# Optimization experiments

Measured on AMD Instinct MI355X. Metric: run time of the kernel, lower is better.

## Reference

```python
import jax, jax.numpy as jnp
import numpy as np

B, S, E, H, DK, DV, DF = 4, 2048, 512, 8, 64, 64, 2048
EPS = 1e-3  # keras LayerNormalization default epsilon


def setup_inputs() -> dict:
    key = jax.random.key(0)
    ks = jax.random.split(key, 24)
    def n(k, shape, scale=0.02):
        return jax.random.normal(k, shape, jnp.float32) * scale
    inp = {}
    inp["x"] = jax.random.normal(ks[0], (B, S, E), jnp.float32)
    inp["encoder_output"] = jax.random.normal(ks[1], (B, S, E), jnp.float32)
    # lookahead mask: 1 above the diagonal (masked), broadcast over batch/heads
    inp["lookahead_mask"] = jnp.triu(jnp.ones((S, S), jnp.int32), k=1)[None, None]
    # padding mask: 0 = keep (no padding in this synthetic batch)
    inp["padding_mask"] = jnp.zeros((B, 1, 1, S), jnp.int32)
    # self-attention params
    inp["sa_Wq"] = n(ks[2], (E, H * DK)); inp["sa_bq"] = jnp.zeros((H * DK,), jnp.float32)
    inp["sa_Wk"] = n(ks[3], (E, H * DK)); inp["sa_bk"] = jnp.zeros((H * DK,), jnp.float32)
    inp["sa_Wv"] = n(ks[4], (E, H * DV)); inp["sa_bv"] = jnp.zeros((H * DV,), jnp.float32)
    inp["sa_Wo"] = n(ks[5], (H * DV, E)); inp["sa_bo"] = jnp.zeros((E,), jnp.float32)
    # cross-attention params
    inp["ca_Wq"] = n(ks[6], (E, H * DK)); inp["ca_bq"] = jnp.zeros((H * DK,), jnp.float32)
    inp["ca_Wk"] = n(ks[7], (E, H * DK)); inp["ca_bk"] = jnp.zeros((H * DK,), jnp.float32)
    inp["ca_Wv"] = n(ks[8], (E, H * DV)); inp["ca_bv"] = jnp.zeros((H * DV,), jnp.float32)
    inp["ca_Wo"] = n(ks[9], (H * DV, E)); inp["ca_bo"] = jnp.zeros((E,), jnp.float32)
    # feed-forward params
    inp["ff_W1"] = n(ks[10], (E, DF)); inp["ff_b1"] = jnp.zeros((DF,), jnp.float32)
    inp["ff_W2"] = n(ks[11], (DF, E)); inp["ff_b2"] = jnp.zeros((E,), jnp.float32)
    # layernorm params (3 add&norm blocks)
    for i in (1, 2, 3):
        inp[f"ln{i}_g"] = jnp.ones((E,), jnp.float32)
        inp[f"ln{i}_b"] = jnp.zeros((E,), jnp.float32)
    return inp


def _mha(q_in, k_in, v_in, mask, Wq, bq, Wk, bk, Wv, bv, Wo, bo):
    Bq, Sq, _ = q_in.shape
    Sk = k_in.shape[1]
    q = (q_in @ Wq + bq).reshape(Bq, Sq, H, DK).transpose(0, 2, 1, 3)  # bhqd
    k = (k_in @ Wk + bk).reshape(Bq, Sk, H, DK).transpose(0, 2, 1, 3)  # bhkd
    v = (v_in @ Wv + bv).reshape(Bq, Sk, H, DV).transpose(0, 2, 1, 3)  # bhkd
    scores = jnp.einsum("bhqd,bhkd->bhqk", q, k) / jnp.sqrt(jnp.float32(DK))
    scores = scores - 1e9 * mask.astype(scores.dtype)  # additive mask (1 = masked)
    attn = jax.nn.softmax(scores, axis=-1)
    out = jnp.einsum("bhqk,bhkd->bhqd", attn, v)
    out = out.transpose(0, 2, 1, 3).reshape(Bq, Sq, H * DV)
    return out @ Wo + bo


def _add_norm(x, sub, g, b):
    y = x + sub
    m = jnp.mean(y, axis=-1, keepdims=True)
    v = jnp.var(y, axis=-1, keepdims=True)
    return (y - m) / jnp.sqrt(v + EPS) * g + b


def reference(x, encoder_output, lookahead_mask, padding_mask,
              sa_Wq, sa_bq, sa_Wk, sa_bk, sa_Wv, sa_bv, sa_Wo, sa_bo,
              ca_Wq, ca_bq, ca_Wk, ca_bk, ca_Wv, ca_bv, ca_Wo, ca_bo,
              ff_W1, ff_b1, ff_W2, ff_b2,
              ln1_g, ln1_b, ln2_g, ln2_b, ln3_g, ln3_b):
    # dropout is identity at inference (training=False)
    a1 = _mha(x, x, x, lookahead_mask,
              sa_Wq, sa_bq, sa_Wk, sa_bk, sa_Wv, sa_bv, sa_Wo, sa_bo)
    x1 = _add_norm(x, a1, ln1_g, ln1_b)
    a2 = _mha(x1, encoder_output, encoder_output, padding_mask,
              ca_Wq, ca_bq, ca_Wk, ca_bk, ca_Wv, ca_bv, ca_Wo, ca_bo)
    x2 = _add_norm(x1, a2, ln2_g, ln2_b)
    ff = jax.nn.relu(x2 @ ff_W1 + ff_b1) @ ff_W2 + ff_b2
    return _add_norm(x2, ff, ln3_g, ln3_b)
```

## Files before the change

kernel.cpp:

```cpp
#include <hip/hip_runtime.h>

#define Bx  4
#define Sx  2048
#define Ex  512
#define Hx  8
#define Tt  (Bx * Sx)

typedef short          short8 __attribute__((ext_vector_type(8)));
typedef float          f32x4  __attribute__((ext_vector_type(4)));
typedef unsigned short u16;

__device__ __forceinline__ u16 f2bf(float f) {
    unsigned int u = __float_as_uint(f);
    u += 0x7fffu + ((u >> 16) & 1u);
    return (u16)(u >> 16);
}
__device__ __forceinline__ float bf2f(u16 h) {
    return __uint_as_float(((unsigned int)h) << 16);
}
__device__ __forceinline__ unsigned int cvt_pk_bf16(float lo, float hi) {
    unsigned int r;
    asm("v_cvt_pk_bf16_f32 %0, %1, %2" : "=v"(r) : "v"(lo), "v"(hi));
    return r;
}
typedef const __attribute__((address_space(1))) void* gas1_t;
typedef __attribute__((address_space(3))) void*       las3_t;
__device__ __forceinline__ void gload16(const u16* g, u16* l) {
    __builtin_amdgcn_global_load_lds((gas1_t)g, (las3_t)l, 16, 0, 0);
}

__global__ __launch_bounds__(256) void f32_to_bf16_2(const float* __restrict__ a,
                                                     const float* __restrict__ b,
                                                     u16* __restrict__ oa,
                                                     u16* __restrict__ ob)
{
    const float* in  = blockIdx.y ? b : a;
    u16*         out = blockIdx.y ? ob : oa;
    int i = (blockIdx.x * 256 + threadIdx.x) << 2;
    float4 v = *(const float4*)(in + i);
    ushort4 o;
    o.x = f2bf(v.x); o.y = f2bf(v.y); o.z = f2bf(v.z); o.w = f2bf(v.w);
    *(ushort4*)(out + i) = o;
}

__global__ __launch_bounds__(256) void transpose_bf16(const float* __restrict__ W,
                                                      u16* __restrict__ Wt,
                                                      int K, int N)
{
    __shared__ u16 tile[32][33];
    const int n0 = blockIdx.x * 32, k0 = blockIdx.y * 32;
    const int tx = threadIdx.x & 31, ty = threadIdx.x >> 5;
#pragma unroll
    for (int i = 0; i < 32; i += 8)
        tile[ty + i][tx] = f2bf(W[(size_t)(k0 + ty + i) * N + n0 + tx]);
    __syncthreads();
#pragma unroll
    for (int i = 0; i < 32; i += 8)
        Wt[(size_t)(n0 + ty + i) * K + k0 + tx] = tile[tx][ty + i];
}

struct WPtrs { const float* w[8]; };
__global__ __launch_bounds__(256) void transpose8_bf16(WPtrs ws, u16* __restrict__ base)
{
    __shared__ u16 tile[32][33];
    const float* W  = ws.w[blockIdx.z];
    u16*         Wt = base + (size_t)blockIdx.z * 262144;
    const int n0 = blockIdx.x * 32, k0 = blockIdx.y * 32;
    const int tx = threadIdx.x & 31, ty = threadIdx.x >> 5;
#pragma unroll
    for (int i = 0; i < 32; i += 8)
        tile[ty + i][tx] = f2bf(W[(size_t)(k0 + ty + i) * 512 + n0 + tx]);
    __syncthreads();
#pragma unroll
    for (int i = 0; i < 32; i += 8)
        Wt[(size_t)(n0 + ty + i) * 512 + k0 + tx] = tile[tx][ty + i];
}

template<int OUT_BF16, int RELU>
__global__ __launch_bounds__(256) void gemm128(const u16* __restrict__ A,
                                               const u16* __restrict__ Bt,
                                               const float* __restrict__ b0,
                                               const float* __restrict__ b1,
                                               const float* __restrict__ b2,
                                               const float* __restrict__ b3,
                                               void* __restrict__ Cout,
                                               int M, int N, int K, int ldc)
{
    __shared__ u16 As[128 * 32];
    __shared__ u16 Bs[128 * 32];

    const int tid  = threadIdx.x;
    const int w    = tid >> 6;
    const int lane = tid & 63;
    const int c    = lane & 15;
    const int quad = lane >> 4;
    const int wr   = w >> 1, wc = w & 1;
    const int m0   = blockIdx.y * 128;
    const int n0   = blockIdx.x * 128;

    const int srow = lane >> 2;
    const int scol = (lane & 3) << 3;
    const u16* Ag0 = A  + (size_t)(m0 + w * 32 + srow) * K + scol;
    const u16* Ag1 = Ag0 + (size_t)16 * K;
    const u16* Bg0 = Bt + (size_t)(n0 + w * 32 + srow) * K + scol;
    const u16* Bg1 = Bg0 + (size_t)16 * K;
    u16* AsB0 = &As[(w * 2 + 0) * 512];
    u16* AsB1 = &As[(w * 2 + 1) * 512];
    u16* BsB0 = &Bs[(w * 2 + 0) * 512];
    u16* BsB1 = &Bs[(w * 2 + 1) * 512];

    f32x4 acc[4][4];
#pragma unroll
    for (int i = 0; i < 4; i++)
#pragma unroll
        for (int j = 0; j < 4; j++) { acc[i][j][0]=0.f; acc[i][j][1]=0.f; acc[i][j][2]=0.f; acc[i][j][3]=0.f; }

    for (int k0 = 0; k0 < K; k0 += 32) {
        __syncthreads();
        gload16(Ag0 + k0, AsB0);
        gload16(Ag1 + k0, AsB1);
        gload16(Bg0 + k0, BsB0);
        gload16(Bg1 + k0, BsB1);
        __syncthreads();

        short8 af[4], bf[4];
#pragma unroll
        for (int i = 0; i < 4; i++)
            af[i] = *(const short8*)&As[(wr * 64 + i * 16 + c) * 32 + quad * 8];
#pragma unroll
        for (int j = 0; j < 4; j++)
            bf[j] = *(const short8*)&Bs[(wc * 64 + j * 16 + c) * 32 + quad * 8];
#pragma unroll
        for (int i = 0; i < 4; i++)
#pragma unroll
            for (int j = 0; j < 4; j++)
                acc[i][j] = __builtin_amdgcn_mfma_f32_16x16x32_bf16(af[i], bf[j], acc[i][j], 0, 0, 0);
    }

    const int seg = n0 >> 9;
    const float* bp = seg == 0 ? b0 : (seg == 1 ? b1 : (seg == 2 ? b2 : b3));
    const int nbase = n0 & 511;
    float bv[4];
#pragma unroll
    for (int j = 0; j < 4; j++) bv[j] = bp[nbase + wc * 64 + j * 16 + c];

#pragma unroll
    for (int i = 0; i < 4; i++) {
#pragma unroll
        for (int j = 0; j < 4; j++) {
            int colg = n0 + wc * 64 + j * 16 + c;
#pragma unroll
            for (int r = 0; r < 4; r++) {
                int rowg = m0 + wr * 64 + i * 16 + quad * 4 + r;
                float v = acc[i][j][r] + bv[j];
                if (RELU) v = fmaxf(v, 0.f);
                if (OUT_BF16) ((u16*)Cout)[(size_t)rowg * ldc + colg] = f2bf(v);
                else          ((float*)Cout)[(size_t)rowg * ldc + colg] = v;
            }
        }
    }
}

template<int OUT_BF16, int RELU>
__global__ __launch_bounds__(128) void gemm64(const u16* __restrict__ A,
                                              const u16* __restrict__ Bt,
                                              const float* __restrict__ bias,
                                              void* __restrict__ Cout,
                                              int M, int N, int K, int ldc)
{
    __shared__ u16 As[128 * 40];
    __shared__ u16 Bs[64 * 40];

    const int tid  = threadIdx.x;
    const int w    = tid >> 6;
    const int lane = tid & 63;
    const int c    = lane & 15;
    const int quad = lane >> 4;
    const int m0   = blockIdx.y * 128;
    const int n0   = blockIdx.x * 64;

    const int rA = tid >> 2;
    const int kc = (tid & 3) << 3;

    const u16* Ap = A  + (size_t)(m0 + rA) * K + kc;
    const u16* Bp = Bt + (size_t)(n0 + rA) * K + kc;
    const size_t a32 = (size_t)32 * K;

    f32x4 acc[4][4];
#pragma unroll
    for (int i = 0; i < 4; i++)
#pragma unroll
        for (int j = 0; j < 4; j++) { acc[i][j][0]=0.f; acc[i][j][1]=0.f; acc[i][j][2]=0.f; acc[i][j][3]=0.f; }

    short8 ra[4], rb[2];
#pragma unroll
    for (int i = 0; i < 4; i++) ra[i] = *(const short8*)(Ap + i * a32);
#pragma unroll
    for (int i = 0; i < 2; i++) rb[i] = *(const short8*)(Bp + i * a32);

    for (int k0 = 0; k0 < K; k0 += 32) {
        __syncthreads();
#pragma unroll
        for (int i = 0; i < 4; i++) *(short8*)&As[(rA + i * 32) * 40 + kc] = ra[i];
#pragma unroll
        for (int i = 0; i < 2; i++) *(short8*)&Bs[(rA + i * 32) * 40 + kc] = rb[i];
        __syncthreads();

        if (k0 + 32 < K) {
#pragma unroll
            for (int i = 0; i < 4; i++) ra[i] = *(const short8*)(Ap + i * a32 + k0 + 32);
#pragma unroll
            for (int i = 0; i < 2; i++) rb[i] = *(const short8*)(Bp + i * a32 + k0 + 32);
        }

        short8 af[4], bf[4];
#pragma unroll
        for (int i = 0; i < 4; i++)
            af[i] = *(const short8*)&As[(w * 64 + i * 16 + c) * 40 + quad * 8];
#pragma unroll
        for (int j = 0; j < 4; j++)
            bf[j] = *(const short8*)&Bs[(j * 16 + c) * 40 + quad * 8];
#pragma unroll
        for (int i = 0; i < 4; i++)
#pragma unroll
            for (int j = 0; j < 4; j++)
                acc[i][j] = __builtin_amdgcn_mfma_f32_16x16x32_bf16(af[i], bf[j], acc[i][j], 0, 0, 0);
    }

    float bv[4];
#pragma unroll
    for (int j = 0; j < 4; j++) bv[j] = bias[n0 + j * 16 + c];

#pragma unroll
    for (int i = 0; i < 4; i++) {
#pragma unroll
        for (int j = 0; j < 4; j++) {
            int colg = n0 + j * 16 + c;
#pragma unroll
            for (int r = 0; r < 4; r++) {
                int rowg = m0 + w * 64 + i * 16 + quad * 4 + r;
                float v = acc[i][j][r] + bv[j];
                if (RELU) v = fmaxf(v, 0.f);
                if (OUT_BF16) ((u16*)Cout)[(size_t)rowg * ldc + colg] = f2bf(v);
                else          ((float*)Cout)[(size_t)rowg * ldc + colg] = v;
            }
        }
    }
}

template<bool CAUSAL>
__global__ __launch_bounds__(256) void attn_mfma(const u16* __restrict__ Q,
                                                 const u16* __restrict__ K,
                                                 const u16* __restrict__ V,
                                                 u16* __restrict__ O,
                                                 int ldq, int ldk, int ldv)
{
    __shared__ u16 Klds[2][64 * 72];
    __shared__ u16 Vtlds[2][64 * 72];

    const int tid  = threadIdx.x;
    const int w    = tid >> 6;
    const int lane = tid & 63;
    const int c    = lane & 15;
    const int quad = lane >> 4;

    const int flat = blockIdx.y * 16 + blockIdx.x;
    const int idx  = flat >> 3;
    const int bh   = (flat & 7) * 4 + (idx >> 4);
    const int q0   = (idx & 15) * 128;

    const int b    = bh >> 3;
    const int h    = bh & 7;
    const int bS   = b * Sx;
    const int hoff = h * 64;
    const int qw   = q0 + w * 32;

    const int kkey = tid >> 3;
    const int kc8  = (tid & 7) << 3;
    const int vdim = tid & 63;
    const int vq   = tid >> 6;
    const int vp   = vq << 3;
    int vkey[8];
#pragma unroll
    for (int j = 0; j < 8; j++) vkey[j] = ((j & 4) << 2) + (vq << 2) + (j & 3);

    short8 qa[2][2];
#pragma unroll
    for (int a = 0; a < 2; a++) {
        const u16* qp = Q + (size_t)(bS + qw + a * 16 + c) * ldq + hoff;
        qa[a][0] = *(const short8*)(qp + quad * 8);
        qa[a][1] = *(const short8*)(qp + 32 + quad * 8);
    }

    f32x4 of[2][4];
#pragma unroll
    for (int a = 0; a < 2; a++)
#pragma unroll
        for (int f = 0; f < 4; f++) { of[a][f][0]=0.f; of[a][f][1]=0.f; of[a][f][2]=0.f; of[a][f][3]=0.f; }
    float lpart[2] = {0.f, 0.f};

    const int kend = CAUSAL ? (q0 + 128) : Sx;

    const u16* Kgp = K + (size_t)(bS + kkey) * ldk + hoff + kc8;
    const u16* Vgp = V + (size_t)bS * ldv + hoff + vdim;
    const size_t k32 = (size_t)32 * ldk;

    {
        short8 kr0 = *(const short8*)(Kgp);
        short8 kr1 = *(const short8*)(Kgp + k32);
        union { short8 v; u16 u[8]; } vb0, vb1;
#pragma unroll
        for (int j = 0; j < 8; j++) vb0.u[j] = Vgp[(size_t)vkey[j] * ldv];
#pragma unroll
        for (int j = 0; j < 8; j++) vb1.u[j] = Vgp[(size_t)(32 + vkey[j]) * ldv];
        *(short8*)&Klds[0][kkey * 72 + kc8]        = kr0;
        *(short8*)&Klds[0][(kkey + 32) * 72 + kc8] = kr1;
        *(short8*)&Vtlds[0][vdim * 72 + vp]        = vb0.v;
        *(short8*)&Vtlds[0][vdim * 72 + 32 + vp]   = vb1.v;
    }
    __syncthreads();

    int cur = 0;
    for (int kt = 0; kt < kend; kt += 64) {
        const bool more = (kt + 64 < kend);

        short8 kr0, kr1;
        union { short8 v; u16 u[8]; } vb0, vb1;
        if (more) {
            const u16* kp = Kgp + (size_t)(kt + 64) * ldk;
            kr0 = *(const short8*)(kp);
            kr1 = *(const short8*)(kp + k32);
#pragma unroll
            for (int j = 0; j < 8; j++)
                vb0.u[j] = Vgp[(size_t)(kt + 64 + vkey[j]) * ldv];
#pragma unroll
            for (int j = 0; j < 8; j++)
                vb1.u[j] = Vgp[(size_t)(kt + 96 + vkey[j]) * ldv];
        }

        int fm0 = 4, fm1 = 4;
        if (CAUSAL) {
            int d0 = ((qw + 15 - kt) >> 4) + 1;
            int d1 = ((qw + 31 - kt) >> 4) + 1;
            fm0 = d0 < 0 ? 0 : (d0 > 4 ? 4 : d0);
            fm1 = d1 < 0 ? 0 : (d1 > 4 ? 4 : d1);
        }

        if (fm1 > 0) {
            f32x4 s[2][4];
#pragma unroll
            for (int f = 0; f < 4; f++) {
                if (f < fm1) {
                    short8 kb0 = *(const short8*)&Klds[cur][(f * 16 + c) * 72 + quad * 8];
                    short8 kb1 = *(const short8*)&Klds[cur][(f * 16 + c) * 72 + 32 + quad * 8];
#pragma unroll
                    for (int a = 0; a < 2; a++) {
                        const int fma_ = a ? fm1 : fm0;
                        if (f < fma_) {
                            f32x4 z; z[0]=0.f; z[1]=0.f; z[2]=0.f; z[3]=0.f;
                            z = __builtin_amdgcn_mfma_f32_16x16x32_bf16(kb0, qa[a][0], z, 0, 0, 0);
                            z = __builtin_amdgcn_mfma_f32_16x16x32_bf16(kb1, qa[a][1], z, 0, 0, 0);
                            s[a][f] = z;
                        }
                    }
                }
            }

            union { unsigned int u[4]; short8 s8; } paA[2], paB[2];
#pragma unroll
            for (int a = 0; a < 2; a++) {
                const int fma_ = a ? fm1 : fm0;
                const int qg = qw + a * 16 + c;
#pragma unroll
                for (int f = 0; f < 4; f++) {
                    float p[4];
#pragma unroll
                    for (int r = 0; r < 4; r++) {
                        float pv = 0.f;
                        int kg = kt + f * 16 + quad * 4 + r;
                        if (f < fma_ && !(CAUSAL && kg > qg))
                            pv = __expf(s[a][f][r] * 0.125f);
                        p[r] = pv;
                    }
                    unsigned int w0 = cvt_pk_bf16(p[0], p[1]);
                    unsigned int w1 = cvt_pk_bf16(p[2], p[3]);
                    lpart[a] += __uint_as_float(w0 << 16) + __uint_as_float(w0 & 0xffff0000u);
                    lpart[a] += __uint_as_float(w1 << 16) + __uint_as_float(w1 & 0xffff0000u);
                    if (f < 2) { paA[a].u[f * 2] = w0; paA[a].u[f * 2 + 1] = w1; }
                    else       { paB[a].u[(f - 2) * 2] = w0; paB[a].u[(f - 2) * 2 + 1] = w1; }
                }
            }

#pragma unroll
            for (int f2 = 0; f2 < 4; f2++) {
                short8 vb0f = *(const short8*)&Vtlds[cur][(f2 * 16 + c) * 72 + quad * 8];
                short8 vb1f = *(const short8*)&Vtlds[cur][(f2 * 16 + c) * 72 + 32 + quad * 8];
                if (fm0 > 0)
                    of[0][f2] = __builtin_amdgcn_mfma_f32_16x16x32_bf16(paA[0].s8, vb0f, of[0][f2], 0, 0, 0);
                of[1][f2] = __builtin_amdgcn_mfma_f32_16x16x32_bf16(paA[1].s8, vb0f, of[1][f2], 0, 0, 0);
                if (fm0 > 2)
                    of[0][f2] = __builtin_amdgcn_mfma_f32_16x16x32_bf16(paB[0].s8, vb1f, of[0][f2], 0, 0, 0);
                if (fm1 > 2)
                    of[1][f2] = __builtin_amdgcn_mfma_f32_16x16x32_bf16(paB[1].s8, vb1f, of[1][f2], 0, 0, 0);
            }
        }

        if (more) {
            *(short8*)&Klds[cur ^ 1][kkey * 72 + kc8]        = kr0;
            *(short8*)&Klds[cur ^ 1][(kkey + 32) * 72 + kc8] = kr1;
            *(short8*)&Vtlds[cur ^ 1][vdim * 72 + vp]        = vb0.v;
            *(short8*)&Vtlds[cur ^ 1][vdim * 72 + 32 + vp]   = vb1.v;
        }
        __syncthreads();
        cur ^= 1;
    }

    float rinv[2][4];
#pragma unroll
    for (int a = 0; a < 2; a++) {
        float D = lpart[a];
        D += __shfl_xor(D, 16, 64);
        D += __shfl_xor(D, 32, 64);
        float rcp = 1.f / D;
#pragma unroll
        for (int r = 0; r < 4; r++)
            rinv[a][r] = __shfl(rcp, quad * 4 + r, 64);
    }

    u16* Ob = O + (size_t)(bS + qw) * Ex + hoff;
#pragma unroll
    for (int a = 0; a < 2; a++)
#pragma unroll
        for (int f = 0; f < 4; f++)
#pragma unroll
            for (int r = 0; r < 4; r++)
                Ob[(size_t)(a * 16 + quad * 4 + r) * Ex + f * 16 + c] =
                    f2bf(of[a][f][r] * rinv[a][r]);
}

__global__ __launch_bounds__(256) void ln_add(const float* __restrict__ x,
                                              const float* __restrict__ s,
                                              const float* __restrict__ g,
                                              const float* __restrict__ bta,
                                              float* __restrict__ out,
                                              u16* __restrict__ out_bf)
{
    __shared__ float red[8];
    const int    row  = blockIdx.x;
    const int    t    = threadIdx.x;
    const size_t base = (size_t)row * Ex;

    float2 xv = *(const float2*)(x + base + (t << 1));
    float2 sv = *(const float2*)(s + base + (t << 1));
    float  y0 = xv.x + sv.x;
    float  y1 = xv.y + sv.y;

    float sum = y0 + y1;
    float sq  = y0 * y0 + y1 * y1;
#pragma unroll
    for (int o = 32; o > 0; o >>= 1) {
        sum += __shfl_down(sum, o, 64);
        sq  += __shfl_down(sq,  o, 64);
    }
    const int wid = t >> 6, lane = t & 63;
    if (lane == 0) { red[wid] = sum; red[4 + wid] = sq; }
    __syncthreads();
    if (t == 0) {
        red[0] = red[0] + red[1] + red[2] + red[3];
        red[4] = red[4] + red[5] + red[6] + red[7];
    }
    __syncthreads();

    const float mean = red[0] * (1.f / 512.f);
    const float var  = red[4] * (1.f / 512.f) - mean * mean;
    const float rstd = rsqrtf(var + 1e-3f);

    float2 gv = *(const float2*)(g   + (t << 1));
    float2 bv = *(const float2*)(bta + (t << 1));
    float  o0 = (y0 - mean) * rstd * gv.x + bv.x;
    float  o1 = (y1 - mean) * rstd * gv.y + bv.y;
    *(float2*)(out + base + (t << 1)) = make_float2(o0, o1);
    if (out_bf) {
        ushort2 ob; ob.x = f2bf(o0); ob.y = f2bf(o1);
        *(ushort2*)(out_bf + base + (t << 1)) = ob;
    }
}

extern "C" void kernel_launch(void* const* d_in, const int* in_sizes, int n_in,
                              void* d_out, int out_size, void* d_ws, size_t ws_size,
                              hipStream_t stream)
{
    const float* x     = (const float*)d_in[0];
    const float* enc   = (const float*)d_in[1];
    const float* sa_Wq = (const float*)d_in[4],  *sa_bq = (const float*)d_in[5];
    const float* sa_Wk = (const float*)d_in[6],  *sa_bk = (const float*)d_in[7];
    const float* sa_Wv = (const float*)d_in[8],  *sa_bv = (const float*)d_in[9];
    const float* sa_Wo = (const float*)d_in[10], *sa_bo = (const float*)d_in[11];
    const float* ca_Wq = (const float*)d_in[12], *ca_bq = (const float*)d_in[13];
    const float* ca_Wk = (const float*)d_in[14], *ca_bk = (const float*)d_in[15];
    const float* ca_Wv = (const float*)d_in[16], *ca_bv = (const float*)d_in[17];
    const float* ca_Wo = (const float*)d_in[18], *ca_bo = (const float*)d_in[19];
    const float* ff_W1 = (const float*)d_in[20], *ff_b1 = (const float*)d_in[21];
    const float* ff_W2 = (const float*)d_in[22], *ff_b2 = (const float*)d_in[23];
    const float* ln1_g = (const float*)d_in[24], *ln1_b = (const float*)d_in[25];
    const float* ln2_g = (const float*)d_in[26], *ln2_b = (const float*)d_in[27];
    const float* ln3_g = (const float*)d_in[28], *ln3_b = (const float*)d_in[29];

    char* ws = (char*)d_ws;
    const size_t MB = 1024 * 1024;
    u16*   bw   = (u16*)(ws);
    u16*   xb   = (u16*)(ws + 8  * MB);
    u16*   encb = (u16*)(ws + 16 * MB);
    u16*   qkvB = (u16*)(ws + 24 * MB);
    u16*   qb   = (u16*)(ws + 24 * MB);
    u16*   kvB  = (u16*)(ws + 32 * MB);
    u16*   ff1b = (u16*)(ws + 24 * MB);
    u16*   ob   = (u16*)(ws + 48 * MB);
    float* projF= (float*)(ws + 56 * MB);
    float* x1f  = (float*)(ws + 72 * MB);
    u16*   x1b  = (u16*)(ws + 88 * MB);
    u16*   x2b  = (u16*)(ws + 88 * MB);
    float* x2f  = (float*)(ws + 8  * MB);

    u16* wsaq = bw;
    u16* wsao = bw + 786432;
    u16* wcaq = bw + 1048576;
    u16* wcak = bw + 1310720;
    u16* wcao = bw + 1835008;
    u16* wff1 = bw + 2097152;
    u16* wff2 = bw + 3145728;

    f32_to_bf16_2<<<dim3(Tt * Ex / 1024, 2), dim3(256), 0, stream>>>(x, enc, xb, encb);
    WPtrs wp; wp.w[0]=sa_Wq; wp.w[1]=sa_Wk; wp.w[2]=sa_Wv; wp.w[3]=sa_Wo;
    wp.w[4]=ca_Wq; wp.w[5]=ca_Wk; wp.w[6]=ca_Wv; wp.w[7]=ca_Wo;
    transpose8_bf16<<<dim3(16, 16, 8), dim3(256), 0, stream>>>(wp, bw);
    transpose_bf16<<<dim3(64, 16), dim3(256), 0, stream>>>(ff_W1, wff1, 512, 2048);
    transpose_bf16<<<dim3(16, 64), dim3(256), 0, stream>>>(ff_W2, wff2, 2048, 512);

    auto G128 = [&](const u16* A, const u16* Wt, const float* b0, const float* b1,
                    const float* b2, const float* b3, void* C,
                    int N, int K, int ldc, int out_bf, int relu) {
        dim3 grid(N / 128, Tt / 128);
        if (out_bf) {
            if (relu) gemm128<1,1><<<grid, dim3(256), 0, stream>>>(A, Wt, b0,b1,b2,b3, C, Tt, N, K, ldc);
            else      gemm128<1,0><<<grid, dim3(256), 0, stream>>>(A, Wt, b0,b1,b2,b3, C, Tt, N, K, ldc);
        } else        gemm128<0,0><<<grid, dim3(256), 0, stream>>>(A, Wt, b0,b1,b2,b3, C, Tt, N, K, ldc);
    };
    auto G64 = [&](const u16* A, const u16* Wt, const float* bi, void* C,
                   int K, int ldc, int out_bf) {
        dim3 grid(512 / 64, Tt / 128);
        if (out_bf) gemm64<1,0><<<grid, dim3(128), 0, stream>>>(A, Wt, bi, C, Tt, 512, K, ldc);
        else        gemm64<0,0><<<grid, dim3(128), 0, stream>>>(A, Wt, bi, C, Tt, 512, K, ldc);
    };
    const dim3 agrid(Sx / 128, Bx * Hx);

    G128(xb, wsaq, sa_bq, sa_bk, sa_bv, sa_bv, qkvB, 1536, 512, 1536, 1, 0);
    attn_mfma<true><<<agrid, dim3(256), 0, stream>>>(qkvB, qkvB + 512, qkvB + 1024,
                                                     ob, 1536, 1536, 1536);
    G64(ob, wsao, sa_bo, projF, 512, 512, 0);
    ln_add<<<dim3(Tt), dim3(256), 0, stream>>>(x, projF, ln1_g, ln1_b, x1f, x1b);

    G64(x1b, wcaq, ca_bq, qb, 512, 512, 1);
    G128(encb, wcak, ca_bk, ca_bv, ca_bv, ca_bv, kvB, 1024, 512, 1024, 1, 0);
    attn_mfma<false><<<agrid, dim3(256), 0, stream>>>(qb, kvB, kvB + 512,
                                                      ob, 512, 1024, 1024);
    G64(ob, wcao, ca_bo, projF, 512, 512, 0);
    ln_add<<<dim3(Tt), dim3(256), 0, stream>>>(x1f, projF, ln2_g, ln2_b, x2f, x2b);

    G128(x2b, wff1, ff_b1, ff_b1 + 512, ff_b1 + 1024, ff_b1 + 1536,
         ff1b, 2048, 512, 2048, 1, 1);
    G64(ff1b, wff2, ff_b2, projF, 2048, 512, 0);
    ln_add<<<dim3(Tt), dim3(256), 0, stream>>>(x2f, projF, ln3_g, ln3_b,
                                               (float*)d_out, (u16*)nullptr);
}
```

Before: 483.8 us.

## Use 4-wave gemm64 with direct LDS loads and row-per-wave LayerNorm

The 128x64 output-tile GEMM now runs four waves of 32 rows each instead of two waves of 64 rows. Tiles are loaded straight into unpadded LDS through the gload16 helper, and the register prefetch of the next k-slice is removed. The add+LayerNorm kernel now handles one row per wave with 8 elements per lane, reducing with xor shuffles and no LDS or block barriers. The aim is more waves per tile and less launch and sync overhead in the LayerNorm, at the cost of losing global-load overlap and possibly adding LDS bank conflicts in the GEMM.

```diff
diff --git a/kernel.cpp b/kernel.cpp
--- a/kernel.cpp
+++ b/kernel.cpp
@@ -162,14 +162,14 @@
 }
 
 template<int OUT_BF16, int RELU>
-__global__ __launch_bounds__(128) void gemm64(const u16* __restrict__ A,
+__global__ __launch_bounds__(256) void gemm64(const u16* __restrict__ A,
                                               const u16* __restrict__ Bt,
                                               const float* __restrict__ bias,
                                               void* __restrict__ Cout,
                                               int M, int N, int K, int ldc)
 {
-    __shared__ u16 As[128 * 40];
-    __shared__ u16 Bs[64 * 40];
+    __shared__ u16 As[128 * 32];
+    __shared__ u16 Bs[64 * 32];
 
     const int tid  = threadIdx.x;
     const int w    = tid >> 6;
@@ -179,49 +179,37 @@
     const int m0   = blockIdx.y * 128;
     const int n0   = blockIdx.x * 64;
 
-    const int rA = tid >> 2;
-    const int kc = (tid & 3) << 3;
-
-    const u16* Ap = A  + (size_t)(m0 + rA) * K + kc;
-    const u16* Bp = Bt + (size_t)(n0 + rA) * K + kc;
-    const size_t a32 = (size_t)32 * K;
-
-    f32x4 acc[4][4];
-#pragma unroll
-    for (int i = 0; i < 4; i++)
+    const int srow = lane >> 2;
+    const int scol = (lane & 3) << 3;
+    const u16* Ag0 = A  + (size_t)(m0 + w * 32 + srow) * K + scol;
+    const u16* Ag1 = Ag0 + (size_t)16 * K;
+    const u16* Bg  = Bt + (size_t)(n0 + w * 16 + srow) * K + scol;
+    u16* AsB0 = &As[(w * 2 + 0) * 512];
+    u16* AsB1 = &As[(w * 2 + 1) * 512];
+    u16* BsB  = &Bs[w * 512];
+
+    f32x4 acc[2][4];
+#pragma unroll
+    for (int i = 0; i < 2; i++)
 #pragma unroll
         for (int j = 0; j < 4; j++) { acc[i][j][0]=0.f; acc[i][j][1]=0.f; acc[i][j][2]=0.f; acc[i][j][3]=0.f; }
-
-    short8 ra[4], rb[2];
-#pragma unroll
-    for (int i = 0; i < 4; i++) ra[i] = *(const short8*)(Ap + i * a32);
-#pragma unroll
-    for (int i = 0; i < 2; i++) rb[i] = *(const short8*)(Bp + i * a32);
 
     for (int k0 = 0; k0 < K; k0 += 32) {
         __syncthreads();
-#pragma unroll
-        for (int i = 0; i < 4; i++) *(short8*)&As[(rA + i * 32) * 40 + kc] = ra[i];
-#pragma unroll
-        for (int i = 0; i < 2; i++) *(short8*)&Bs[(rA + i * 32) * 40 + kc] = rb[i];
+        gload16(Ag0 + k0, AsB0);
+        gload16(Ag1 + k0, AsB1);
+        gload16(Bg  + k0, BsB);
         __syncthreads();
 
-        if (k0 + 32 < K) {
-#pragma unroll
-            for (int i = 0; i < 4; i++) ra[i] = *(const short8*)(Ap + i * a32 + k0 + 32);
-#pragma unroll
-            for (int i = 0; i < 2; i++) rb[i] = *(const short8*)(Bp + i * a32 + k0 + 32);
-        }
-
-        short8 af[4], bf[4];
-#pragma unroll
-        for (int i = 0; i < 4; i++)
-            af[i] = *(const short8*)&As[(w * 64 + i * 16 + c) * 40 + quad * 8];
+        short8 af[2], bf[4];
+#pragma unroll
+        for (int i = 0; i < 2; i++)
+            af[i] = *(const short8*)&As[(w * 32 + i * 16 + c) * 32 + quad * 8];
 #pragma unroll
         for (int j = 0; j < 4; j++)
-            bf[j] = *(const short8*)&Bs[(j * 16 + c) * 40 + quad * 8];
-#pragma unroll
-        for (int i = 0; i < 4; i++)
+            bf[j] = *(const short8*)&Bs[(j * 16 + c) * 32 + quad * 8];
+#pragma unroll
+        for (int i = 0; i < 2; i++)
 #pragma unroll
             for (int j = 0; j < 4; j++)
                 acc[i][j] = __builtin_amdgcn_mfma_f32_16x16x32_bf16(af[i], bf[j], acc[i][j], 0, 0, 0);
@@ -232,13 +220,13 @@
     for (int j = 0; j < 4; j++) bv[j] = bias[n0 + j * 16 + c];
 
 #pragma unroll
-    for (int i = 0; i < 4; i++) {
+    for (int i = 0; i < 2; i++) {
 #pragma unroll
         for (int j = 0; j < 4; j++) {
             int colg = n0 + j * 16 + c;
 #pragma unroll
             for (int r = 0; r < 4; r++) {
-                int rowg = m0 + w * 64 + i * 16 + quad * 4 + r;
+                int rowg = m0 + w * 32 + i * 16 + quad * 4 + r;
                 float v = acc[i][j][r] + bv[j];
                 if (RELU) v = fmaxf(v, 0.f);
                 if (OUT_BF16) ((u16*)Cout)[(size_t)rowg * ldc + colg] = f2bf(v);
@@ -445,44 +433,51 @@
                                               float* __restrict__ out,
                                               u16* __restrict__ out_bf)
 {
-    __shared__ float red[8];
-    const int    row  = blockIdx.x;
-    const int    t    = threadIdx.x;
-    const size_t base = (size_t)row * Ex;
-
-    float2 xv = *(const float2*)(x + base + (t << 1));
-    float2 sv = *(const float2*)(s + base + (t << 1));
-    float  y0 = xv.x + sv.x;
-    float  y1 = xv.y + sv.y;
-
-    float sum = y0 + y1;
-    float sq  = y0 * y0 + y1 * y1;
-#pragma unroll
-    for (int o = 32; o > 0; o >>= 1) {
-        sum += __shfl_down(sum, o, 64);
-        sq  += __shfl_down(sq,  o, 64);
-    }
-    const int wid = t >> 6, lane = t & 63;
-    if (lane == 0) { red[wid] = sum; red[4 + wid] = sq; }
-    __syncthreads();
-    if (t == 0) {
-        red[0] = red[0] + red[1] + red[2] + red[3];
-        red[4] = red[4] + red[5] + red[6] + red[7];
-    }
-    __syncthreads();
-
-    const float mean = red[0] * (1.f / 512.f);
-    const float var  = red[4] * (1.f / 512.f) - mean * mean;
+    const int t    = threadIdx.x;
+    const int w    = t >> 6;
+    const int lane = t & 63;
+    const int row  = blockIdx.x * 4 + w;
+    const size_t base = (size_t)row * Ex + lane * 8;
+    const int    gi   = lane * 8;
+
+    float4 xv0 = *(const float4*)(x + base);
+    float4 xv1 = *(const float4*)(x + base + 4);
+    float4 sv0 = *(const float4*)(s + base);
+    float4 sv1 = *(const float4*)(s + base + 4);
+    float y[8] = { xv0.x + sv0.x, xv0.y + sv0.y, xv0.z + sv0.z, xv0.w + sv0.w,
+                   xv1.x + sv1.x, xv1.y + sv1.y, xv1.z + sv1.z, xv1.w + sv1.w };
+
+    float sum = 0.f, sq = 0.f;
+#pragma unroll
+    for (int i = 0; i < 8; i++) { sum += y[i]; sq += y[i] * y[i]; }
+#pragma unroll
+    for (int o = 1; o < 64; o <<= 1) {
+        sum += __shfl_xor(sum, o, 64);
+        sq  += __shfl_xor(sq,  o, 64);
+    }
+
+    const float mean = sum * (1.f / 512.f);
+    const float var  = sq * (1.f / 512.f) - mean * mean;
     const float rstd = rsqrtf(var + 1e-3f);
 
-    float2 gv = *(const float2*)(g   + (t << 1));
-    float2 bv = *(const float2*)(bta + (t << 1));
-    float  o0 = (y0 - mean) * rstd * gv.x + bv.x;
-    float  o1 = (y1 - mean) * rstd * gv.y + bv.y;
-    *(float2*)(out + base + (t << 1)) = make_float2(o0, o1);
+    float4 gv0 = *(const float4*)(g + gi);
+    float4 gv1 = *(const float4*)(g + gi + 4);
+    float4 bv0 = *(const float4*)(bta + gi);
+    float4 bv1 = *(const float4*)(bta + gi + 4);
+    float gg[8] = { gv0.x, gv0.y, gv0.z, gv0.w, gv1.x, gv1.y, gv1.z, gv1.w };
+    float bb[8] = { bv0.x, bv0.y, bv0.z, bv0.w, bv1.x, bv1.y, bv1.z, bv1.w };
+
+    float o8[8];
+#pragma unroll
+    for (int i = 0; i < 8; i++) o8[i] = (y[i] - mean) * rstd * gg[i] + bb[i];
+
+    *(float4*)(out + base)     = make_float4(o8[0], o8[1], o8[2], o8[3]);
+    *(float4*)(out + base + 4) = make_float4(o8[4], o8[5], o8[6], o8[7]);
     if (out_bf) {
-        ushort2 ob; ob.x = f2bf(o0); ob.y = f2bf(o1);
-        *(ushort2*)(out_bf + base + (t << 1)) = ob;
+        union { short8 v; u16 u[8]; } ob;
+#pragma unroll
+        for (int i = 0; i < 8; i++) ob.u[i] = f2bf(o8[i]);
+        *(short8*)(out_bf + base) = ob.v;
     }
 }
 
@@ -549,27 +544,28 @@
     auto G64 = [&](const u16* A, const u16* Wt, const float* bi, void* C,
                    int K, int ldc, int out_bf) {
         dim3 grid(512 / 64, Tt / 128);
-        if (out_bf) gemm64<1,0><<<grid, dim3(128), 0, stream>>>(A, Wt, bi, C, Tt, 512, K, ldc);
-        else        gemm64<0,0><<<grid, dim3(128), 0, stream>>>(A, Wt, bi, C, Tt, 512, K, ldc);
+        if (out_bf) gemm64<1,0><<<grid, dim3(256), 0, stream>>>(A, Wt, bi, C, Tt, 512, K, ldc);
+        else        gemm64<0,0><<<grid, dim3(256), 0, stream>>>(A, Wt, bi, C, Tt, 512, K, ldc);
     };
     const dim3 agrid(Sx / 128, Bx * Hx);
+    const dim3 lgrid(Tt / 4);
 
     G128(xb, wsaq, sa_bq, sa_bk, sa_bv, sa_bv, qkvB, 1536, 512, 1536, 1, 0);
     attn_mfma<true><<<agrid, dim3(256), 0, stream>>>(qkvB, qkvB + 512, qkvB + 1024,
                                                      ob, 1536, 1536, 1536);
     G64(ob, wsao, sa_bo, projF, 512, 512, 0);
-    ln_add<<<dim3(Tt), dim3(256), 0, stream>>>(x, projF, ln1_g, ln1_b, x1f, x1b);
+    ln_add<<<lgrid, dim3(256), 0, stream>>>(x, projF, ln1_g, ln1_b, x1f, x1b);
 
     G64(x1b, wcaq, ca_bq, qb, 512, 512, 1);
     G128(encb, wcak, ca_bk, ca_bv, ca_bv, ca_bv, kvB, 1024, 512, 1024, 1, 0);
     attn_mfma<false><<<agrid, dim3(256), 0, stream>>>(qb, kvB, kvB + 512,
                                                       ob, 512, 1024, 1024);
     G64(ob, wcao, ca_bo, projF, 512, 512, 0);
-    ln_add<<<dim3(Tt), dim3(256), 0, stream>>>(x1f, projF, ln2_g, ln2_b, x2f, x2b);
+    ln_add<<<lgrid, dim3(256), 0, stream>>>(x1f, projF, ln2_g, ln2_b, x2f, x2b);
 
     G128(x2b, wff1, ff_b1, ff_b1 + 512, ff_b1 + 1024, ff_b1 + 1536,
          ff1b, 2048, 512, 2048, 1, 1);
     G64(ff1b, wff2, ff_b2, projF, 2048, 512, 0);
-    ln_add<<<dim3(Tt), dim3(256), 0, stream>>>(x2f, projF, ln3_g, ln3_b,
-                                               (float*)d_out, (u16*)nullptr);
-}
+    ln_add<<<lgrid, dim3(256), 0, stream>>>(x2f, projF, ln3_g, ln3_b,
+                                            (float*)d_out, (u16*)nullptr);
+}
```

Result: no change. 482.1 us (-0.3%).
